# Kernel tuning notes

Hardware: AMD Instinct MI355X
Metric: run time of the kernel (lower is better)

Reference implementation:

```python
import jax, jax.numpy as jnp
import numpy as np

B, C_IN, C_OUT, N = 8, 256, 128, 4096
BN_EPS = 1e-5


def _conv1x1(w, b, t):
    # w: [out, in], t: [B, in, N] -> [B, out, N]
    return jnp.einsum('oc,bcn->bon', w, t) + b[None, :, None]


def setup_inputs() -> dict:
    key = jax.random.key(0)
    ks = jax.random.split(key, 11)
    s_in = 1.0 / np.sqrt(C_IN)
    s_out = 1.0 / np.sqrt(C_OUT)
    return {
        'x': jax.random.normal(ks[0], (B, C_IN, N), dtype=jnp.float32),
        'g_w': jax.random.normal(ks[1], (C_OUT, C_IN), dtype=jnp.float32) * s_in,
        'g_b': jax.random.normal(ks[2], (C_OUT,), dtype=jnp.float32) * s_in,
        'theta_w': jax.random.normal(ks[3], (C_OUT, C_IN), dtype=jnp.float32) * s_in,
        'theta_b': jax.random.normal(ks[4], (C_OUT,), dtype=jnp.float32) * s_in,
        'phi_w': jax.random.normal(ks[5], (C_OUT, C_IN), dtype=jnp.float32) * s_in,
        'phi_b': jax.random.normal(ks[6], (C_OUT,), dtype=jnp.float32) * s_in,
        'W_w': jax.random.normal(ks[7], (C_IN, C_OUT), dtype=jnp.float32) * s_out,
        'W_b': jax.random.normal(ks[8], (C_IN,), dtype=jnp.float32) * s_out,
        'bn_gamma': jax.random.uniform(ks[9], (C_IN,), dtype=jnp.float32),
        'bn_beta': jax.random.normal(ks[10], (C_IN,), dtype=jnp.float32) * 0.1,
    }


def reference(x, g_w, g_b, theta_w, theta_b, phi_w, phi_b, W_w, W_b, bn_gamma, bn_beta):
    n = x.shape[-1]
    g_x = _conv1x1(g_w, g_b, x)          # [B, Co, N]
    theta_x = _conv1x1(theta_w, theta_b, x)  # [B, Co, N]
    phi_x = _conv1x1(phi_w, phi_b, x)        # [B, Co, N]
    # f = theta_x^T @ phi_x, divided by N (no softmax) -> [B, N, N]
    f_div_c = jnp.einsum('bcn,bcm->bnm', theta_x, phi_x) / n
    # y[b,c,n] = sum_m f[b,n,m] * g_x[b,c,m]  -> already permuted to [B, Co, N]
    y = jnp.einsum('bnm,bcm->bcn', f_div_c, g_x)
    w_y = jnp.einsum('oc,bcn->bon', W_w, y) + W_b[None, :, None]  # [B, C_in, N]
    # BatchNorm1d, training mode: stats over (batch, spatial), biased variance
    mean = w_y.mean(axis=(0, 2), keepdims=True)
    var = w_y.var(axis=(0, 2), keepdims=True)
    w_y = (w_y - mean) * jax.lax.rsqrt(var + BN_EPS)
    w_y = w_y * bn_gamma[None, :, None] + bn_beta[None, :, None]
    return w_y + x  # generate=True residual
```

## Files before the change

kernel.cpp:

```cpp
#include <hip/hip_runtime.h>
#include <hip/hip_bf16.h>
#include <stdint.h>

#define BB   8
#define CIN  256
#define COUT 128
#define NN   4096

using f32x4  = __attribute__((ext_vector_type(4))) float;
using bf16x8 = __attribute__((ext_vector_type(8))) __bf16;
using u16x8  = __attribute__((ext_vector_type(8))) unsigned short;

static __device__ __forceinline__ unsigned short f2bf(float f) {
    unsigned int u = __builtin_bit_cast(unsigned int, f);
    u += 0x7FFFu + ((u >> 16) & 1u);
    return (unsigned short)(u >> 16);
}
static __device__ __forceinline__ float bf2f(unsigned short u) {
    return __builtin_bit_cast(float, (unsigned int)u << 16);
}
static __device__ __forceinline__ ushort4 pack4(float a, float b, float c, float d) {
    ushort4 r; r.x=f2bf(a); r.y=f2bf(b); r.z=f2bf(c); r.w=f2bf(d); return r;
}
static __device__ __forceinline__ bf16x8 pack8(float4 a, float4 b) {
    u16x8 r;
    r[0]=f2bf(a.x); r[1]=f2bf(a.y); r[2]=f2bf(a.z); r[3]=f2bf(a.w);
    r[4]=f2bf(b.x); r[5]=f2bf(b.y); r[6]=f2bf(b.z); r[7]=f2bf(b.w);
    return __builtin_bit_cast(bf16x8, r);
}
#define MFMA(a,b,c) __builtin_amdgcn_mfma_f32_16x16x32_bf16((a),(b),(c),0,0,0)

static __device__ __forceinline__ int sw64(int r, int c)  { return (r*64  + c) ^ ((r&7)<<3); }

typedef __attribute__((address_space(3))) unsigned int lds_uint;
typedef __attribute__((address_space(1))) const unsigned int glob_uint;
static __device__ __forceinline__ void glds16(const void* g, void* l) {
    __builtin_amdgcn_global_load_lds((glob_uint*)g, (lds_uint*)l, 16, 0, 0);
}

__global__ __launch_bounds__(256) void z0_prep(
    const float* __restrict__ gw, const float* __restrict__ pw, const float* __restrict__ tw,
    const float* __restrict__ gb, const float* __restrict__ pb, const float* __restrict__ tb,
    float* __restrict__ stats,
    unsigned short* __restrict__ Wcat, float* __restrict__ biascat)
{
    int t = blockIdx.x * 256 + threadIdx.x;
    int gs = gridDim.x * 256;
    for (int i = t; i < 24576; i += gs) {
        int flat = i * 4;
        int o = flat >> 8, c = flat & 255;
        const float* src = (o < 128) ? (gw + o*256) : (o < 256) ? (pw + (o-128)*256) : (tw + (o-256)*256);
        float4 f = *(const float4*)(src + c);
        ushort4 u; u.x=f2bf(f.x); u.y=f2bf(f.y); u.z=f2bf(f.z); u.w=f2bf(f.w);
        *(ushort4*)(Wcat + flat) = u;
    }
    if (t < 512) stats[t] = 0.f;
    if (t < 384)
        biascat[t] = (t < 128) ? gb[t] : (t < 256) ? pb[t-128] : tb[t-256];
}

__global__ __launch_bounds__(512) void k1_conv3(
    const float* __restrict__ x, const unsigned short* __restrict__ Wcat,
    const float* __restrict__ biascat,
    unsigned short* __restrict__ G, unsigned short* __restrict__ P,
    unsigned short* __restrict__ TT)
{
    __shared__ __align__(16) unsigned short Xs[128*256];
    int b  = blockIdx.x >> 5;
    int n0 = (blockIdx.x & 31) * 128;
    int t  = threadIdx.x;

    {
        int nq = (t & 31) * 4;
        int c0 = (t >> 5) * 4;
        const float* xb = x + (size_t)b*CIN*NN + n0 + nq;
        #pragma unroll
        for (int p = 0; p < 4; ++p) {
            int c = p*64 + c0;
            const float* xp = xb + (size_t)c*NN;
            float4 f0 = *(const float4*)(xp);
            float4 f1 = *(const float4*)(xp + NN);
            float4 f2 = *(const float4*)(xp + 2*NN);
            float4 f3 = *(const float4*)(xp + 3*NN);
            *(ushort4*)&Xs[(nq+0)*256 + (c ^ (((nq+0)&7)<<3))] = pack4(f0.x,f1.x,f2.x,f3.x);
            *(ushort4*)&Xs[(nq+1)*256 + (c ^ (((nq+1)&7)<<3))] = pack4(f0.y,f1.y,f2.y,f3.y);
            *(ushort4*)&Xs[(nq+2)*256 + (c ^ (((nq+2)&7)<<3))] = pack4(f0.z,f1.z,f2.z,f3.z);
            *(ushort4*)&Xs[(nq+3)*256 + (c ^ (((nq+3)&7)<<3))] = pack4(f0.w,f1.w,f2.w,f3.w);
        }
    }
    __syncthreads();

    int lane = t & 63, wv = t >> 6;
    int wr = wv >> 2, wc = wv & 3;
    int lr = lane & 15, lg = lane >> 4;
    int nb = wr*64, ob = wc*96;

    f32x4 acc[4][6];
    #pragma unroll
    for (int i=0;i<4;i++)
        #pragma unroll
        for (int j=0;j<6;j++) acc[i][j] = (f32x4){0.f,0.f,0.f,0.f};

    #pragma unroll
    for (int ks = 0; ks < 8; ++ks) {
        bf16x8 xf[4], wf[6];
        #pragma unroll
        for (int ni = 0; ni < 4; ++ni) {
            int n = nb + ni*16 + lr;
            int cq = (ks*4 + lg) ^ (n & 7);
            xf[ni] = __builtin_bit_cast(bf16x8, *(const u16x8*)&Xs[n*256 + cq*8]);
        }
        #pragma unroll
        for (int os = 0; os < 6; ++os) {
            int o = ob + os*16 + lr;
            wf[os] = __builtin_bit_cast(bf16x8, *(const u16x8*)(Wcat + (size_t)o*256 + ks*32 + lg*8));
        }
        #pragma unroll
        for (int os = 0; os < 6; ++os) {
            bool th = (ob + os*16) >= 256;
            #pragma unroll
            for (int ni = 0; ni < 4; ++ni)
                acc[ni][os] = th ? MFMA(wf[os], xf[ni], acc[ni][os])
                                 : MFMA(xf[ni], wf[os], acc[ni][os]);
        }
    }

    unsigned short* Gb  = G  + (size_t)b*COUT*NN;
    unsigned short* Pb  = P  + (size_t)b*COUT*NN;
    unsigned short* TTb = TT + (size_t)b*NN*COUT;
    #pragma unroll
    for (int os = 0; os < 6; ++os) {
        int o = ob + os*16;
        if (o < 256) {
            float bv = biascat[o + lr];
            unsigned short* dst = ((o < 128) ? (Gb + (size_t)(o + lr)*NN)
                                             : (Pb + (size_t)(o - 128 + lr)*NN)) + n0 + nb;
            #pragma unroll
            for (int ni = 0; ni < 4; ++ni) {
                f32x4 v = acc[ni][os];
                *(ushort4*)(dst + ni*16 + lg*4) = pack4(v[0]+bv, v[1]+bv, v[2]+bv, v[3]+bv);
            }
        } else {
            int c0 = o - 256 + lg*4;
            float b0 = biascat[o + lg*4 + 0];
            float b1 = biascat[o + lg*4 + 1];
            float b2 = biascat[o + lg*4 + 2];
            float b3 = biascat[o + lg*4 + 3];
            #pragma unroll
            for (int ni = 0; ni < 4; ++ni) {
                int n = n0 + nb + ni*16 + lr;
                f32x4 v = acc[ni][os];
                *(ushort4*)(TTb + (size_t)n*COUT + c0) = pack4(v[0]+b0, v[1]+b1, v[2]+b2, v[3]+b3);
            }
        }
    }
}

__global__ __launch_bounds__(256) void k2_m1(
    const unsigned short* __restrict__ P, const unsigned short* __restrict__ G,
    float* __restrict__ M1p)
{
    __shared__ __align__(16) unsigned short Ps[128*64];
    __shared__ __align__(16) unsigned short Gs[128*64];
    int bid = blockIdx.x;
    int b  = bid >> 4;
    int ks = bid & 15;
    int t = threadIdx.x;
    int lane = t & 63, wv = t >> 6;
    int wr = wv >> 1, wc = wv & 1;
    int lr = lane & 15, lg = lane >> 4;

    f32x4 acc[4][4];
    #pragma unroll
    for (int i=0;i<4;i++)
        #pragma unroll
        for (int j=0;j<4;j++) acc[i][j] = (f32x4){0.f,0.f,0.f,0.f};

    const unsigned short* Pb = P + (size_t)b*COUT*NN;
    const unsigned short* Gb = G + (size_t)b*COUT*NN;

    for (int it = 0; it < 4; ++it) {
        int n0 = ks*256 + it*64;
        #pragma unroll
        for (int g4 = 0; g4 < 4; ++g4) {
            int row0 = wv*32 + g4*8;
            int row  = row0 + (lane >> 3);
            int gg   = (lane & 7) ^ (row & 7);
            glds16(Pb + (size_t)row*NN + n0 + gg*8, &Ps[row0*64]);
            glds16(Gb + (size_t)row*NN + n0 + gg*8, &Gs[row0*64]);
        }
        asm volatile("s_waitcnt vmcnt(0)");
        __syncthreads();
        #pragma unroll
        for (int kk = 0; kk < 2; ++kk) {
            bf16x8 af[4], bfr[4];
            #pragma unroll
            for (int mi=0; mi<4; ++mi) {
                int row = wr*64 + mi*16 + lr;
                af[mi] = __builtin_bit_cast(bf16x8, *(const u16x8*)&Ps[sw64(row, kk*32 + lg*8)]);
            }
            #pragma unroll
            for (int ni=0; ni<4; ++ni) {
                int row = wc*64 + ni*16 + lr;
                bfr[ni] = __builtin_bit_cast(bf16x8, *(const u16x8*)&Gs[sw64(row, kk*32 + lg*8)]);
            }
            #pragma unroll
            for (int mi=0; mi<4; ++mi)
                #pragma unroll
                for (int ni=0; ni<4; ++ni)
                    acc[mi][ni] = MFMA(af[mi], bfr[ni], acc[mi][ni]);
        }
        __syncthreads();
    }
    float* dst = M1p + (size_t)bid*16384;
    #pragma unroll
    for (int mi=0; mi<4; ++mi)
        #pragma unroll
        for (int j=0; j<4; ++j) {
            int kch = wr*64 + mi*16 + lg*4 + j;
            #pragma unroll
            for (int ni=0; ni<4; ++ni) {
                int cch = wc*64 + ni*16 + lr;
                dst[kch*128 + cch] = acc[mi][ni][j];
            }
        }
}

__global__ __launch_bounds__(512) void k3_w2(
    const float* __restrict__ Ww, const float* __restrict__ M1p,
    unsigned short* __restrict__ W2)
{
    __shared__ float Ms[16384];
    int b = blockIdx.x;
    int t = threadIdx.x;

    for (int i4 = t; i4 < 4096; i4 += 512) {
        float4 s = {0.f,0.f,0.f,0.f};
        #pragma unroll
        for (int p = 0; p < 16; ++p) {
            float4 v = ((const float4*)(M1p + (size_t)(b*16 + p)*16384))[i4];
            s.x += v.x; s.y += v.y; s.z += v.z; s.w += v.w;
        }
        int k = i4 >> 5, q = i4 & 31;
        *(float4*)&Ms[k*128 + ((q ^ (k&7)) * 4)] = s;
    }
    __syncthreads();

    int lane = t & 63, wv = t >> 6;
    int lr = lane & 15, lg = lane >> 4;
    #pragma unroll
    for (int oo = 0; oo < 2; ++oo) {
        int o16 = oo*128 + wv*16;
        bf16x8 a[4];
        const float* wrow = Ww + (size_t)(o16 + lr)*128;
        #pragma unroll
        for (int ksx=0; ksx<4; ++ksx) {
            float4 f0 = *(const float4*)(wrow + ksx*32 + lg*8);
            float4 f1 = *(const float4*)(wrow + ksx*32 + lg*8 + 4);
            a[ksx] = pack8(f0, f1);
        }
        for (int kt = 0; kt < 8; ++kt) {
            f32x4 acc = (f32x4){0.f,0.f,0.f,0.f};
            int k = kt*16 + lr;
            #pragma unroll
            for (int ksx=0; ksx<4; ++ksx) {
                int q0 = ksx*8 + lg*2;
                float4 f0 = *(const float4*)&Ms[k*128 + ((q0     ^ (k&7)) * 4)];
                float4 f1 = *(const float4*)&Ms[k*128 + (((q0+1) ^ (k&7)) * 4)];
                acc = MFMA(a[ksx], pack8(f0, f1), acc);
            }
            #pragma unroll
            for (int j=0;j<4;++j) {
                int o = o16 + lg*4 + j;
                W2[(size_t)b*32768 + (size_t)o*128 + (kt*16 + lr)] = f2bf(acc[j] * (1.0f/4096.0f));
            }
        }
    }
}

__global__ __launch_bounds__(512) void k4_wy(
    const unsigned short* __restrict__ W2, const unsigned short* __restrict__ TT,
    const float* __restrict__ Wb, unsigned short* __restrict__ WY,
    float* __restrict__ stats)
{
    __shared__ __align__(16) unsigned short Ts[128*128];
    __shared__ float sb[512];
    int b  = blockIdx.x >> 5;
    int n0 = (blockIdx.x & 31) * 128;
    int t  = threadIdx.x;
    int lane = t & 63, wv = t >> 6;
    sb[t] = 0.f;

    const unsigned short* TTb = TT + ((size_t)b*NN + n0)*COUT;
    #pragma unroll
    for (int g = 0; g < 4; ++g) {
        int nl = wv*16 + g*4 + (lane >> 4);
        int kq = lane & 15;
        const unsigned short* src = TTb + (size_t)nl*128 + ((kq ^ (nl & 7)) * 8);
        glds16(src, &Ts[(wv*16 + g*4) * 128]);
    }
    asm volatile("s_waitcnt vmcnt(0)");
    __syncthreads();

    int wr = wv >> 2, wo = wv & 3;
    int lr = lane & 15, lg = lane >> 4;
    int nb = wr*64, ob = wo*64;
    const unsigned short* W2b = W2 + (size_t)b*32768;

    f32x4 acc[4][4];
    #pragma unroll
    for (int i=0;i<4;i++)
        #pragma unroll
        for (int j=0;j<4;j++) acc[i][j] = (f32x4){0.f,0.f,0.f,0.f};

    #pragma unroll
    for (int ks = 0; ks < 4; ++ks) {
        bf16x8 tf[4], wf[4];
        #pragma unroll
        for (int ni = 0; ni < 4; ++ni) {
            int n = nb + ni*16 + lr;
            int kq = (ks*4 + lg) ^ (n & 7);
            tf[ni] = __builtin_bit_cast(bf16x8, *(const u16x8*)&Ts[n*128 + kq*8]);
        }
        #pragma unroll
        for (int oi = 0; oi < 4; ++oi) {
            int o = ob + oi*16 + lr;
            wf[oi] = __builtin_bit_cast(bf16x8, *(const u16x8*)(W2b + (size_t)o*128 + ks*32 + lg*8));
        }
        #pragma unroll
        for (int ni = 0; ni < 4; ++ni)
            #pragma unroll
            for (int oi = 0; oi < 4; ++oi)
                acc[ni][oi] = MFMA(tf[ni], wf[oi], acc[ni][oi]);
    }

    unsigned short* wyb = WY + (size_t)b*CIN*NN;
    #pragma unroll
    for (int oi = 0; oi < 4; ++oi) {
        int o = ob + oi*16 + lr;
        float bv = Wb[o];
        float s1 = 0.f, s2 = 0.f;
        #pragma unroll
        for (int ni = 0; ni < 4; ++ni) {
            f32x4 v = acc[ni][oi];
            float v0 = v[0]+bv, v1 = v[1]+bv, v2 = v[2]+bv, v3 = v[3]+bv;
            s1 += v0+v1+v2+v3;
            s2 += v0*v0+v1*v1+v2*v2+v3*v3;
            *(ushort4*)(wyb + (size_t)o*NN + n0 + nb + ni*16 + lg*4) = pack4(v0,v1,v2,v3);
        }
        s1 += __shfl_xor(s1, 16); s1 += __shfl_xor(s1, 32);
        s2 += __shfl_xor(s2, 16); s2 += __shfl_xor(s2, 32);
        if (lg == 0) {
            atomicAdd(&sb[o], s1);
            atomicAdd(&sb[256 + o], s2);
        }
    }
    __syncthreads();
    atomicAdd(&stats[t], sb[t]);
}

__global__ __launch_bounds__(256) void k6_final(
    const unsigned short* __restrict__ WY, const float* __restrict__ x,
    const float* __restrict__ stats, const float* __restrict__ gamma,
    const float* __restrict__ beta, float* __restrict__ out)
{
    const float inv = 1.0f / (float)(BB * NN);
    int stride = gridDim.x * blockDim.x;
    for (int i = blockIdx.x * blockDim.x + threadIdx.x; i < (BB*CIN*NN)/8; i += stride) {
        int c = (i >> 9) & 255;
        float mean = stats[c] * inv;
        float var  = stats[256 + c] * inv - mean*mean;
        float sc   = gamma[c] * rsqrtf(var + 1e-5f);
        float bb   = beta[c];
        u16x8 w = ((const u16x8*)WY)[i];
        float4 x0 = ((const float4*)x)[i*2];
        float4 x1 = ((const float4*)x)[i*2+1];
        float4 r0, r1;
        r0.x = (bf2f(w[0]) - mean)*sc + bb + x0.x;
        r0.y = (bf2f(w[1]) - mean)*sc + bb + x0.y;
        r0.z = (bf2f(w[2]) - mean)*sc + bb + x0.z;
        r0.w = (bf2f(w[3]) - mean)*sc + bb + x0.w;
        r1.x = (bf2f(w[4]) - mean)*sc + bb + x1.x;
        r1.y = (bf2f(w[5]) - mean)*sc + bb + x1.y;
        r1.z = (bf2f(w[6]) - mean)*sc + bb + x1.z;
        r1.w = (bf2f(w[7]) - mean)*sc + bb + x1.w;
        ((float4*)out)[i*2]   = r0;
        ((float4*)out)[i*2+1] = r1;
    }
}

extern "C" void kernel_launch(void* const* d_in, const int* in_sizes, int n_in,
                              void* d_out, int out_size, void* d_ws, size_t ws_size,
                              hipStream_t stream)
{
    (void)in_sizes; (void)n_in; (void)out_size; (void)ws_size;
    const float* x     = (const float*)d_in[0];
    const float* gw    = (const float*)d_in[1];
    const float* gb    = (const float*)d_in[2];
    const float* tw    = (const float*)d_in[3];
    const float* tb    = (const float*)d_in[4];
    const float* pw    = (const float*)d_in[5];
    const float* pb    = (const float*)d_in[6];
    const float* Ww    = (const float*)d_in[7];
    const float* Wb    = (const float*)d_in[8];
    const float* gamma = (const float*)d_in[9];
    const float* beta  = (const float*)d_in[10];
    float* out = (float*)d_out;

    char* ws = (char*)d_ws;
    unsigned short* G    = (unsigned short*)(ws + 0);
    unsigned short* P    = (unsigned short*)(ws + (8u<<20));
    unsigned short* WY   = (unsigned short*)(ws + 0);
    unsigned short* TT   = (unsigned short*)(ws + (16u<<20));
    float* M1p           = (float*)(ws + (24u<<20));
    unsigned short* W2   = (unsigned short*)(ws + (32u<<20));
    unsigned short* Wcat = (unsigned short*)(ws + (33u<<20));
    float* biascat       = (float*)(ws + (33u<<20) + 196608);
    float* stats         = (float*)(ws + (33u<<20) + 198656);

    z0_prep <<<96,   256, 0, stream>>>(gw, pw, tw, gb, pb, tb, stats, Wcat, biascat);
    k1_conv3<<<256,  512, 0, stream>>>(x, Wcat, biascat, G, P, TT);
    k2_m1   <<<128,  256, 0, stream>>>(P, G, M1p);
    k3_w2   <<<8,    512, 0, stream>>>(Ww, M1p, W2);
    k4_wy   <<<256,  512, 0, stream>>>(W2, TT, Wb, WY, stats);
    k6_final<<<2048, 256, 0, stream>>>(WY, x, stats, gamma, beta, out);
}
```

Before: 96.35 us.

## Refactor nonlocal block via per-batch Gram matrix of x and closed-form BN stats

Replaces the conv/attention pipeline with an algebraic reformulation. Each batch's Gram matrix X·Xᵀ and channel sums of x are computed once. All 1x1 weights are folded into a single per-batch 256x256 effective matrix E, so the output becomes E·x plus a bias. BatchNorm statistics are derived analytically from E, the Gram matrix and the row sums, so no intermediate activation tensor is written. This removes the large G/P/TT/WY round trips, at the cost of fp32 partial-Gram traffic and a serial 8-block small-matrix stage, with different bf16 rounding behavior.

```diff
diff --git a/kernel.cpp b/kernel.cpp
--- a/kernel.cpp
+++ b/kernel.cpp
@@ -22,57 +22,397 @@
 static __device__ __forceinline__ ushort4 pack4(float a, float b, float c, float d) {
     ushort4 r; r.x=f2bf(a); r.y=f2bf(b); r.z=f2bf(c); r.w=f2bf(d); return r;
 }
-static __device__ __forceinline__ bf16x8 pack8(float4 a, float4 b) {
-    u16x8 r;
-    r[0]=f2bf(a.x); r[1]=f2bf(a.y); r[2]=f2bf(a.z); r[3]=f2bf(a.w);
-    r[4]=f2bf(b.x); r[5]=f2bf(b.y); r[6]=f2bf(b.z); r[7]=f2bf(b.w);
-    return __builtin_bit_cast(bf16x8, r);
-}
 #define MFMA(a,b,c) __builtin_amdgcn_mfma_f32_16x16x32_bf16((a),(b),(c),0,0,0)
 
-static __device__ __forceinline__ int sw64(int r, int c)  { return (r*64  + c) ^ ((r&7)<<3); }
-
-typedef __attribute__((address_space(3))) unsigned int lds_uint;
-typedef __attribute__((address_space(1))) const unsigned int glob_uint;
-static __device__ __forceinline__ void glds16(const void* g, void* l) {
-    __builtin_amdgcn_global_load_lds((glob_uint*)g, (lds_uint*)l, 16, 0, 0);
-}
-
-__global__ __launch_bounds__(256) void z0_prep(
-    const float* __restrict__ gw, const float* __restrict__ pw, const float* __restrict__ tw,
-    const float* __restrict__ gb, const float* __restrict__ pb, const float* __restrict__ tb,
-    float* __restrict__ stats,
-    unsigned short* __restrict__ Wcat, float* __restrict__ biascat)
+__global__ __launch_bounds__(512) void kA_gram(
+    const float* __restrict__ x, float* __restrict__ Sp, float* __restrict__ Rp)
 {
-    int t = blockIdx.x * 256 + threadIdx.x;
-    int gs = gridDim.x * 256;
-    for (int i = t; i < 24576; i += gs) {
-        int flat = i * 4;
-        int o = flat >> 8, c = flat & 255;
-        const float* src = (o < 128) ? (gw + o*256) : (o < 256) ? (pw + (o-128)*256) : (tw + (o-256)*256);
-        float4 f = *(const float4*)(src + c);
-        ushort4 u; u.x=f2bf(f.x); u.y=f2bf(f.y); u.z=f2bf(f.z); u.w=f2bf(f.w);
-        *(ushort4*)(Wcat + flat) = u;
-    }
-    if (t < 512) stats[t] = 0.f;
-    if (t < 384)
-        biascat[t] = (t < 128) ? gb[t] : (t < 256) ? pb[t-128] : tb[t-256];
-}
-
-__global__ __launch_bounds__(512) void k1_conv3(
-    const float* __restrict__ x, const unsigned short* __restrict__ Wcat,
-    const float* __restrict__ biascat,
-    unsigned short* __restrict__ G, unsigned short* __restrict__ P,
-    unsigned short* __restrict__ TT)
+    __shared__ __align__(16) unsigned short Xs[256*256];
+    int bid = blockIdx.x;
+    int b = bid >> 4, ch = bid & 15;
+    int n0 = ch * 256;
+    int t = threadIdx.x, lane = t & 63, wv = t >> 6;
+
+    const float* xb = x + (size_t)b*CIN*NN + n0;
+    #pragma unroll
+    for (int i = 0; i < 32; ++i) {
+        int c = wv*32 + i;
+        float4 f = *(const float4*)(xb + (size_t)c*NN + lane*4);
+        float s = f.x + f.y + f.z + f.w;
+        #pragma unroll
+        for (int off = 1; off < 64; off <<= 1) s += __shfl_xor(s, off);
+        if (lane == 0) Rp[bid*256 + c] = s;
+        *(ushort4*)&Xs[(c*256 + lane*4) ^ ((c&7)<<3)] = pack4(f.x, f.y, f.z, f.w);
+    }
+    __syncthreads();
+
+    int wr = wv >> 1, wc = wv & 1;
+    int lr = lane & 15, lg = lane >> 4;
+    f32x4 acc[4][8];
+    #pragma unroll
+    for (int i = 0; i < 4; ++i)
+        #pragma unroll
+        for (int j = 0; j < 8; ++j) acc[i][j] = (f32x4){0.f,0.f,0.f,0.f};
+
+    #pragma unroll
+    for (int ks = 0; ks < 8; ++ks) {
+        bf16x8 af[4], bfr[8];
+        #pragma unroll
+        for (int mi = 0; mi < 4; ++mi) {
+            int row = wr*64 + mi*16 + lr;
+            af[mi] = __builtin_bit_cast(bf16x8, *(const u16x8*)&Xs[(row*256 + ks*32 + lg*8) ^ ((row&7)<<3)]);
+        }
+        #pragma unroll
+        for (int ni = 0; ni < 8; ++ni) {
+            int row = wc*128 + ni*16 + lr;
+            bfr[ni] = __builtin_bit_cast(bf16x8, *(const u16x8*)&Xs[(row*256 + ks*32 + lg*8) ^ ((row&7)<<3)]);
+        }
+        #pragma unroll
+        for (int mi = 0; mi < 4; ++mi)
+            #pragma unroll
+            for (int ni = 0; ni < 8; ++ni)
+                acc[mi][ni] = MFMA(af[mi], bfr[ni], acc[mi][ni]);
+    }
+
+    float* dst = Sp + (size_t)bid * 65536;
+    #pragma unroll
+    for (int mi = 0; mi < 4; ++mi)
+        #pragma unroll
+        for (int ni = 0; ni < 8; ++ni)
+            #pragma unroll
+            for (int j = 0; j < 4; ++j) {
+                int c1 = wr*64 + mi*16 + lg*4 + j;
+                int c2 = wc*128 + ni*16 + lr;
+                dst[c1*256 + c2] = acc[mi][ni][j];
+            }
+}
+
+__global__ __launch_bounds__(256) void kR(
+    const float* __restrict__ Sp, const float* __restrict__ Rp,
+    const float* __restrict__ pw, const float* __restrict__ gw,
+    const float* __restrict__ tw, const float* __restrict__ Www,
+    unsigned short* __restrict__ Sbf, float* __restrict__ rv,
+    unsigned short* __restrict__ Pwb, unsigned short* __restrict__ Gwb,
+    unsigned short* __restrict__ TwT, unsigned short* __restrict__ Wwb,
+    float* __restrict__ stats)
+{
+    int blk = blockIdx.x, t = threadIdx.x;
+    if (blk < 128) {
+        int b = blk >> 4, part = blk & 15;
+        int base = part * 4096;
+        #pragma unroll
+        for (int i4 = t; i4 < 1024; i4 += 256) {
+            float4 s = {0.f,0.f,0.f,0.f};
+            #pragma unroll
+            for (int p = 0; p < 16; ++p) {
+                float4 v = *(const float4*)(Sp + (size_t)(b*16+p)*65536 + base + i4*4);
+                s.x += v.x; s.y += v.y; s.z += v.z; s.w += v.w;
+            }
+            *(ushort4*)(Sbf + (size_t)b*65536 + base + i4*4) = pack4(s.x, s.y, s.z, s.w);
+        }
+    } else if (blk < 136) {
+        int b = blk - 128;
+        float s = 0.f;
+        #pragma unroll
+        for (int p = 0; p < 16; ++p) s += Rp[(b*16+p)*256 + t];
+        rv[b*256 + t] = s;
+    } else {
+        int j = (blk - 136)*256 + t;
+        for (int i = j; i < 32768; i += 2048) {
+            Pwb[i] = f2bf(pw[i]);
+            Gwb[i] = f2bf(gw[i]);
+            Wwb[i] = f2bf(Www[i]);
+            int c = i >> 7, k = i & 127;
+            TwT[i] = f2bf(tw[k*256 + c]);
+        }
+        if (blk == 136) stats[t] = 0.f;
+        if (blk == 137) stats[256 + t] = 0.f;
+    }
+}
+
+__global__ __launch_bounds__(512) void kB12(
+    const unsigned short* __restrict__ Sbf, const float* __restrict__ rv,
+    const float* __restrict__ pwf, const float* __restrict__ gwf,
+    const unsigned short* __restrict__ Pwb, const unsigned short* __restrict__ Gwb,
+    const unsigned short* __restrict__ TwT, const unsigned short* __restrict__ Wwb,
+    const float* __restrict__ gbv, const float* __restrict__ pbv,
+    const float* __restrict__ tbv, const float* __restrict__ Wbv,
+    unsigned short* __restrict__ Ebf, float* __restrict__ fv)
+{
+    __shared__ __align__(16) unsigned short Ss[128*256];
+    __shared__ __align__(16) unsigned short Tbuf[128*128];
+    __shared__ float u_l[128], v_l[128], pb_l[128], gb_l[128];
+    int b = blockIdx.x, t = threadIdx.x, lane = t & 63, wv = t >> 6;
+    int lr = lane & 15, lg = lane >> 4;
+    const unsigned short* Sb = Sbf + (size_t)b*65536;
+    const float* rb = rv + b*256;
+
+    if (t < 128) {
+        float s = 0.f;
+        for (int c = 0; c < 256; ++c) s += pwf[t*256 + c] * rb[c];
+        u_l[t] = s; pb_l[t] = pbv[t];
+    } else if (t < 256) {
+        int k = t - 128;
+        float s = 0.f;
+        for (int c = 0; c < 256; ++c) s += gwf[k*256 + c] * rb[c];
+        v_l[k] = s; gb_l[k] = gbv[k];
+    }
+
+    int wrM = wv >> 2, wcM = wv & 3;
+    f32x4 accM[4][2];
+    #pragma unroll
+    for (int i = 0; i < 4; ++i) { accM[i][0] = (f32x4){0,0,0,0}; accM[i][1] = (f32x4){0,0,0,0}; }
+
+    for (int h = 0; h < 2; ++h) {
+        __syncthreads();
+        for (int i = t; i < 4096; i += 512) {
+            int row = i >> 5, c8 = (i & 31) * 8;
+            u16x8 vv = *(const u16x8*)(Sb + (size_t)(h*128 + row)*256 + c8);
+            *(u16x8*)&Ss[(row*256 + c8) ^ ((row&7)<<3)] = vv;
+        }
+        __syncthreads();
+        f32x4 accT[4][2];
+        #pragma unroll
+        for (int i = 0; i < 4; ++i) { accT[i][0] = (f32x4){0,0,0,0}; accT[i][1] = (f32x4){0,0,0,0}; }
+        #pragma unroll
+        for (int ks = 0; ks < 8; ++ks) {
+            bf16x8 a4[4], b2[2];
+            #pragma unroll
+            for (int mi = 0; mi < 4; ++mi) {
+                int k = wrM*64 + mi*16 + lr;
+                a4[mi] = __builtin_bit_cast(bf16x8, *(const u16x8*)(Pwb + (size_t)k*256 + ks*32 + lg*8));
+            }
+            #pragma unroll
+            for (int ni = 0; ni < 2; ++ni) {
+                int c2l = wcM*32 + ni*16 + lr;
+                b2[ni] = __builtin_bit_cast(bf16x8, *(const u16x8*)&Ss[(c2l*256 + ks*32 + lg*8) ^ ((c2l&7)<<3)]);
+            }
+            #pragma unroll
+            for (int mi = 0; mi < 4; ++mi)
+                #pragma unroll
+                for (int ni = 0; ni < 2; ++ni)
+                    accT[mi][ni] = MFMA(a4[mi], b2[ni], accT[mi][ni]);
+        }
+        __syncthreads();
+        #pragma unroll
+        for (int mi = 0; mi < 4; ++mi)
+            #pragma unroll
+            for (int ni = 0; ni < 2; ++ni)
+                #pragma unroll
+                for (int j = 0; j < 4; ++j) {
+                    int k = wrM*64 + mi*16 + lg*4 + j;
+                    int c2l = wcM*32 + ni*16 + lr;
+                    Tbuf[(k*128 + c2l) ^ ((k&7)<<3)] = f2bf(accT[mi][ni][j]);
+                }
+        __syncthreads();
+        #pragma unroll
+        for (int ks = 0; ks < 4; ++ks) {
+            bf16x8 a4[4], b2[2];
+            #pragma unroll
+            for (int mi = 0; mi < 4; ++mi) {
+                int k = wrM*64 + mi*16 + lr;
+                a4[mi] = __builtin_bit_cast(bf16x8, *(const u16x8*)&Tbuf[(k*128 + ks*32 + lg*8) ^ ((k&7)<<3)]);
+            }
+            #pragma unroll
+            for (int ni = 0; ni < 2; ++ni) {
+                int c = wcM*32 + ni*16 + lr;
+                b2[ni] = __builtin_bit_cast(bf16x8, *(const u16x8*)(Gwb + (size_t)c*256 + h*128 + ks*32 + lg*8));
+            }
+            #pragma unroll
+            for (int mi = 0; mi < 4; ++mi)
+                #pragma unroll
+                for (int ni = 0; ni < 2; ++ni)
+                    accM[mi][ni] = MFMA(a4[mi], b2[ni], accM[mi][ni]);
+        }
+    }
+    __syncthreads();
+    #pragma unroll
+    for (int mi = 0; mi < 4; ++mi)
+        #pragma unroll
+        for (int ni = 0; ni < 2; ++ni)
+            #pragma unroll
+            for (int j = 0; j < 4; ++j) {
+                int k = wrM*64 + mi*16 + lg*4 + j;
+                int c = wcM*32 + ni*16 + lr;
+                float val = accM[mi][ni][j] + u_l[k]*gb_l[c] + pb_l[k]*v_l[c] + 4096.0f*pb_l[k]*gb_l[c];
+                Tbuf[(k*128 + c) ^ ((k&7)<<3)] = f2bf(val);
+            }
+    __syncthreads();
+    int wrW = wv >> 1, wcW = wv & 1;
+    f32x4 accW[4][4];
+    #pragma unroll
+    for (int i = 0; i < 4; ++i)
+        #pragma unroll
+        for (int j = 0; j < 4; ++j) accW[i][j] = (f32x4){0,0,0,0};
+    #pragma unroll
+    for (int ks = 0; ks < 4; ++ks) {
+        bf16x8 a4[4], b4[4];
+        #pragma unroll
+        for (int mi = 0; mi < 4; ++mi) {
+            int o = wrW*64 + mi*16 + lr;
+            a4[mi] = __builtin_bit_cast(bf16x8, *(const u16x8*)(Wwb + (size_t)o*128 + ks*32 + lg*8));
+        }
+        #pragma unroll
+        for (int ni = 0; ni < 4; ++ni) {
+            int kk = wcW*64 + ni*16 + lr;
+            b4[ni] = __builtin_bit_cast(bf16x8, *(const u16x8*)&Tbuf[(kk*128 + ks*32 + lg*8) ^ ((kk&7)<<3)]);
+        }
+        #pragma unroll
+        for (int mi = 0; mi < 4; ++mi)
+            #pragma unroll
+            for (int ni = 0; ni < 4; ++ni)
+                accW[mi][ni] = MFMA(a4[mi], b4[ni], accW[mi][ni]);
+    }
+    __syncthreads();
+    #pragma unroll
+    for (int mi = 0; mi < 4; ++mi)
+        #pragma unroll
+        for (int ni = 0; ni < 4; ++ni)
+            #pragma unroll
+            for (int j = 0; j < 4; ++j) {
+                int o = wrW*64 + mi*16 + lg*4 + j;
+                int kk = wcW*64 + ni*16 + lr;
+                Ss[(o*128 + kk) ^ ((o&7)<<3)] = f2bf(accW[mi][ni][j] * (1.0f/4096.0f));
+            }
+    __syncthreads();
+    f32x4 accE[4][8];
+    #pragma unroll
+    for (int i = 0; i < 4; ++i)
+        #pragma unroll
+        for (int j = 0; j < 8; ++j) accE[i][j] = (f32x4){0,0,0,0};
+    #pragma unroll
+    for (int ks = 0; ks < 4; ++ks) {
+        bf16x8 a4[4], b8[8];
+        #pragma unroll
+        for (int mi = 0; mi < 4; ++mi) {
+            int o = wrW*64 + mi*16 + lr;
+            a4[mi] = __builtin_bit_cast(bf16x8, *(const u16x8*)&Ss[(o*128 + ks*32 + lg*8) ^ ((o&7)<<3)]);
+        }
+        #pragma unroll
+        for (int ni = 0; ni < 8; ++ni) {
+            int cp = wcW*128 + ni*16 + lr;
+            b8[ni] = __builtin_bit_cast(bf16x8, *(const u16x8*)(TwT + (size_t)cp*128 + ks*32 + lg*8));
+        }
+        #pragma unroll
+        for (int mi = 0; mi < 4; ++mi)
+            #pragma unroll
+            for (int ni = 0; ni < 8; ++ni)
+                accE[mi][ni] = MFMA(a4[mi], b8[ni], accE[mi][ni]);
+    }
+    unsigned short* Eb = Ebf + (size_t)b*65536;
+    #pragma unroll
+    for (int mi = 0; mi < 4; ++mi)
+        #pragma unroll
+        for (int ni = 0; ni < 8; ++ni)
+            #pragma unroll
+            for (int j = 0; j < 4; ++j) {
+                int o = wrW*64 + mi*16 + lg*4 + j;
+                int cp = wcW*128 + ni*16 + lr;
+                Eb[(size_t)o*256 + cp] = f2bf(accE[mi][ni][j]);
+            }
+    if (t < 256) {
+        float s = 0.f;
+        for (int kk = 0; kk < 128; ++kk)
+            s += bf2f(Ss[(t*128 + kk) ^ ((t&7)<<3)]) * tbv[kk];
+        fv[b*256 + t] = s + Wbv[t];
+    }
+}
+
+__global__ __launch_bounds__(256) void kB3(
+    const unsigned short* __restrict__ Ebf, const unsigned short* __restrict__ Sbf,
+    const float* __restrict__ rv, const float* __restrict__ fv, float* __restrict__ stats)
+{
+    __shared__ __align__(16) unsigned short Es[64*256];
+    __shared__ float s2l[64];
+    __shared__ float er4[256];
+    int b = blockIdx.x >> 2, sl = blockIdx.x & 3, obase = sl*64;
+    int t = threadIdx.x, lane = t & 63, wv = t >> 6, lr = lane & 15, lg = lane >> 4;
+    const unsigned short* Eb = Ebf + (size_t)b*65536;
+    const unsigned short* Sb = Sbf + (size_t)b*65536;
+
+    for (int i = t; i < 2048; i += 256) {
+        int row = i >> 5, c8 = (i & 31) * 8;
+        u16x8 vv = *(const u16x8*)(Eb + (size_t)(obase + row)*256 + c8);
+        *(u16x8*)&Es[(row*256 + c8) ^ ((row&7)<<3)] = vv;
+    }
+    if (t < 64) s2l[t] = 0.f;
+    __syncthreads();
+
+    f32x4 acc[4][4];
+    #pragma unroll
+    for (int i = 0; i < 4; ++i)
+        #pragma unroll
+        for (int j = 0; j < 4; ++j) acc[i][j] = (f32x4){0,0,0,0};
+    #pragma unroll
+    for (int ks = 0; ks < 8; ++ks) {
+        bf16x8 a4[4], b4[4];
+        #pragma unroll
+        for (int mi = 0; mi < 4; ++mi) {
+            int ol = mi*16 + lr;
+            a4[mi] = __builtin_bit_cast(bf16x8, *(const u16x8*)&Es[(ol*256 + ks*32 + lg*8) ^ ((ol&7)<<3)]);
+        }
+        #pragma unroll
+        for (int ni = 0; ni < 4; ++ni) {
+            int c2 = wv*64 + ni*16 + lr;
+            b4[ni] = __builtin_bit_cast(bf16x8, *(const u16x8*)(Sb + (size_t)c2*256 + ks*32 + lg*8));
+        }
+        #pragma unroll
+        for (int mi = 0; mi < 4; ++mi)
+            #pragma unroll
+            for (int ni = 0; ni < 4; ++ni)
+                acc[mi][ni] = MFMA(a4[mi], b4[ni], acc[mi][ni]);
+    }
+    #pragma unroll
+    for (int mi = 0; mi < 4; ++mi)
+        #pragma unroll
+        for (int j = 0; j < 4; ++j) {
+            int ol = mi*16 + lg*4 + j;
+            float v = 0.f;
+            #pragma unroll
+            for (int ni = 0; ni < 4; ++ni) {
+                int c2 = wv*64 + ni*16 + lr;
+                v += acc[mi][ni][j] * bf2f(Es[(ol*256 + c2) ^ ((ol&7)<<3)]);
+            }
+            v += __shfl_xor(v, 1); v += __shfl_xor(v, 2);
+            v += __shfl_xor(v, 4); v += __shfl_xor(v, 8);
+            if (lr == 0) atomicAdd(&s2l[ol], v);
+        }
+    {
+        int ol = t & 63, q = t >> 6;
+        float p = 0.f;
+        for (int c = q*64; c < q*64 + 64; ++c)
+            p += bf2f(Es[(ol*256 + c) ^ ((ol&7)<<3)]) * rv[b*256 + c];
+        er4[q*64 + ol] = p;
+    }
+    __syncthreads();
+    if (t < 64) {
+        float er = er4[t] + er4[64+t] + er4[128+t] + er4[192+t];
+        float fo = fv[b*256 + obase + t];
+        atomicAdd(&stats[obase + t], er + 4096.0f*fo);
+        atomicAdd(&stats[256 + obase + t], s2l[t] + 2.0f*fo*er + 4096.0f*fo*fo);
+    }
+}
+
+__global__ __launch_bounds__(512) void kF(
+    const float* __restrict__ x, const unsigned short* __restrict__ Ebf,
+    const float* __restrict__ fv, const float* __restrict__ stats,
+    const float* __restrict__ gamma, const float* __restrict__ beta,
+    float* __restrict__ out)
 {
     __shared__ __align__(16) unsigned short Xs[128*256];
-    int b  = blockIdx.x >> 5;
-    int n0 = (blockIdx.x & 31) * 128;
-    int t  = threadIdx.x;
-
+    __shared__ float scale_l[256], shift_l[256];
+    int b = blockIdx.x >> 5, n0 = (blockIdx.x & 31) * 128;
+    int t = threadIdx.x, lane = t & 63, wv = t >> 6, lr = lane & 15, lg = lane >> 4;
+    const float inv = 1.0f / 32768.0f;
+    if (t < 256) {
+        float mu  = stats[t] * inv;
+        float var = stats[256 + t] * inv - mu*mu;
+        float sc  = gamma[t] * rsqrtf(var + 1e-5f);
+        scale_l[t] = sc;
+        shift_l[t] = (fv[b*256 + t] - mu) * sc + beta[t];
+    }
     {
-        int nq = (t & 31) * 4;
-        int c0 = (t >> 5) * 4;
+        int nq = (t & 31) * 4, c0 = (t >> 5) * 4;
         const float* xb = x + (size_t)b*CIN*NN + n0 + nq;
         #pragma unroll
         for (int p = 0; p < 4; ++p) {
@@ -90,302 +430,52 @@
     }
     __syncthreads();
 
-    int lane = t & 63, wv = t >> 6;
-    int wr = wv >> 2, wc = wv & 3;
-    int lr = lane & 15, lg = lane >> 4;
-    int nb = wr*64, ob = wc*96;
-
-    f32x4 acc[4][6];
-    #pragma unroll
-    for (int i=0;i<4;i++)
-        #pragma unroll
-        for (int j=0;j<6;j++) acc[i][j] = (f32x4){0.f,0.f,0.f,0.f};
+    int wn = wv >> 2, wo = wv & 3;
+    int nb = wn*64, ob = wo*64;
+    const unsigned short* Eb = Ebf + (size_t)b*65536;
+    f32x4 acc[4][4];
+    #pragma unroll
+    for (int i = 0; i < 4; ++i)
+        #pragma unroll
+        for (int j = 0; j < 4; ++j) acc[i][j] = (f32x4){0,0,0,0};
 
     #pragma unroll
     for (int ks = 0; ks < 8; ++ks) {
-        bf16x8 xf[4], wf[6];
+        bf16x8 xf[4], ef[4];
         #pragma unroll
         for (int ni = 0; ni < 4; ++ni) {
             int n = nb + ni*16 + lr;
-            int cq = (ks*4 + lg) ^ (n & 7);
-            xf[ni] = __builtin_bit_cast(bf16x8, *(const u16x8*)&Xs[n*256 + cq*8]);
-        }
-        #pragma unroll
-        for (int os = 0; os < 6; ++os) {
-            int o = ob + os*16 + lr;
-            wf[os] = __builtin_bit_cast(bf16x8, *(const u16x8*)(Wcat + (size_t)o*256 + ks*32 + lg*8));
-        }
-        #pragma unroll
-        for (int os = 0; os < 6; ++os) {
-            bool th = (ob + os*16) >= 256;
-            #pragma unroll
-            for (int ni = 0; ni < 4; ++ni)
-                acc[ni][os] = th ? MFMA(wf[os], xf[ni], acc[ni][os])
-                                 : MFMA(xf[ni], wf[os], acc[ni][os]);
-        }
-    }
-
-    unsigned short* Gb  = G  + (size_t)b*COUT*NN;
-    unsigned short* Pb  = P  + (size_t)b*COUT*NN;
-    unsigned short* TTb = TT + (size_t)b*NN*COUT;
-    #pragma unroll
-    for (int os = 0; os < 6; ++os) {
-        int o = ob + os*16;
-        if (o < 256) {
-            float bv = biascat[o + lr];
-            unsigned short* dst = ((o < 128) ? (Gb + (size_t)(o + lr)*NN)
-                                             : (Pb + (size_t)(o - 128 + lr)*NN)) + n0 + nb;
-            #pragma unroll
-            for (int ni = 0; ni < 4; ++ni) {
-                f32x4 v = acc[ni][os];
-                *(ushort4*)(dst + ni*16 + lg*4) = pack4(v[0]+bv, v[1]+bv, v[2]+bv, v[3]+bv);
-            }
-        } else {
-            int c0 = o - 256 + lg*4;
-            float b0 = biascat[o + lg*4 + 0];
-            float b1 = biascat[o + lg*4 + 1];
-            float b2 = biascat[o + lg*4 + 2];
-            float b3 = biascat[o + lg*4 + 3];
-            #pragma unroll
-            for (int ni = 0; ni < 4; ++ni) {
-                int n = n0 + nb + ni*16 + lr;
-                f32x4 v = acc[ni][os];
-                *(ushort4*)(TTb + (size_t)n*COUT + c0) = pack4(v[0]+b0, v[1]+b1, v[2]+b2, v[3]+b3);
-            }
-        }
-    }
-}
-
-__global__ __launch_bounds__(256) void k2_m1(
-    const unsigned short* __restrict__ P, const unsigned short* __restrict__ G,
-    float* __restrict__ M1p)
-{
-    __shared__ __align__(16) unsigned short Ps[128*64];
-    __shared__ __align__(16) unsigned short Gs[128*64];
-    int bid = blockIdx.x;
-    int b  = bid >> 4;
-    int ks = bid & 15;
-    int t = threadIdx.x;
-    int lane = t & 63, wv = t >> 6;
-    int wr = wv >> 1, wc = wv & 1;
-    int lr = lane & 15, lg = lane >> 4;
-
-    f32x4 acc[4][4];
-    #pragma unroll
-    for (int i=0;i<4;i++)
-        #pragma unroll
-        for (int j=0;j<4;j++) acc[i][j] = (f32x4){0.f,0.f,0.f,0.f};
-
-    const unsigned short* Pb = P + (size_t)b*COUT*NN;
-    const unsigned short* Gb = G + (size_t)b*COUT*NN;
-
-    for (int it = 0; it < 4; ++it) {
-        int n0 = ks*256 + it*64;
-        #pragma unroll
-        for (int g4 = 0; g4 < 4; ++g4) {
-            int row0 = wv*32 + g4*8;
-            int row  = row0 + (lane >> 3);
-            int gg   = (lane & 7) ^ (row & 7);
-            glds16(Pb + (size_t)row*NN + n0 + gg*8, &Ps[row0*64]);
-            glds16(Gb + (size_t)row*NN + n0 + gg*8, &Gs[row0*64]);
-        }
-        asm volatile("s_waitcnt vmcnt(0)");
-        __syncthreads();
-        #pragma unroll
-        for (int kk = 0; kk < 2; ++kk) {
-            bf16x8 af[4], bfr[4];
-            #pragma unroll
-            for (int mi=0; mi<4; ++mi) {
-                int row = wr*64 + mi*16 + lr;
-                af[mi] = __builtin_bit_cast(bf16x8, *(const u16x8*)&Ps[sw64(row, kk*32 + lg*8)]);
-            }
-            #pragma unroll
-            for (int ni=0; ni<4; ++ni) {
-                int row = wc*64 + ni*16 + lr;
-                bfr[ni] = __builtin_bit_cast(bf16x8, *(const u16x8*)&Gs[sw64(row, kk*32 + lg*8)]);
-            }
-            #pragma unroll
-            for (int mi=0; mi<4; ++mi)
-                #pragma unroll
-                for (int ni=0; ni<4; ++ni)
-                    acc[mi][ni] = MFMA(af[mi], bfr[ni], acc[mi][ni]);
-        }
-        __syncthreads();
-    }
-    float* dst = M1p + (size_t)bid*16384;
-    #pragma unroll
-    for (int mi=0; mi<4; ++mi)
-        #pragma unroll
-        for (int j=0; j<4; ++j) {
-            int kch = wr*64 + mi*16 + lg*4 + j;
-            #pragma unroll
-            for (int ni=0; ni<4; ++ni) {
-                int cch = wc*64 + ni*16 + lr;
-                dst[kch*128 + cch] = acc[mi][ni][j];
-            }
-        }
-}
-
-__global__ __launch_bounds__(512) void k3_w2(
-    const float* __restrict__ Ww, const float* __restrict__ M1p,
-    unsigned short* __restrict__ W2)
-{
-    __shared__ float Ms[16384];
-    int b = blockIdx.x;
-    int t = threadIdx.x;
-
-    for (int i4 = t; i4 < 4096; i4 += 512) {
-        float4 s = {0.f,0.f,0.f,0.f};
-        #pragma unroll
-        for (int p = 0; p < 16; ++p) {
-            float4 v = ((const float4*)(M1p + (size_t)(b*16 + p)*16384))[i4];
-            s.x += v.x; s.y += v.y; s.z += v.z; s.w += v.w;
-        }
-        int k = i4 >> 5, q = i4 & 31;
-        *(float4*)&Ms[k*128 + ((q ^ (k&7)) * 4)] = s;
-    }
-    __syncthreads();
-
-    int lane = t & 63, wv = t >> 6;
-    int lr = lane & 15, lg = lane >> 4;
-    #pragma unroll
-    for (int oo = 0; oo < 2; ++oo) {
-        int o16 = oo*128 + wv*16;
-        bf16x8 a[4];
-        const float* wrow = Ww + (size_t)(o16 + lr)*128;
-        #pragma unroll
-        for (int ksx=0; ksx<4; ++ksx) {
-            float4 f0 = *(const float4*)(wrow + ksx*32 + lg*8);
-            float4 f1 = *(const float4*)(wrow + ksx*32 + lg*8 + 4);
-            a[ksx] = pack8(f0, f1);
-        }
-        for (int kt = 0; kt < 8; ++kt) {
-            f32x4 acc = (f32x4){0.f,0.f,0.f,0.f};
-            int k = kt*16 + lr;
-            #pragma unroll
-            for (int ksx=0; ksx<4; ++ksx) {
-                int q0 = ksx*8 + lg*2;
-                float4 f0 = *(const float4*)&Ms[k*128 + ((q0     ^ (k&7)) * 4)];
-                float4 f1 = *(const float4*)&Ms[k*128 + (((q0+1) ^ (k&7)) * 4)];
-                acc = MFMA(a[ksx], pack8(f0, f1), acc);
-            }
-            #pragma unroll
-            for (int j=0;j<4;++j) {
-                int o = o16 + lg*4 + j;
-                W2[(size_t)b*32768 + (size_t)o*128 + (kt*16 + lr)] = f2bf(acc[j] * (1.0f/4096.0f));
-            }
-        }
-    }
-}
-
-__global__ __launch_bounds__(512) void k4_wy(
-    const unsigned short* __restrict__ W2, const unsigned short* __restrict__ TT,
-    const float* __restrict__ Wb, unsigned short* __restrict__ WY,
-    float* __restrict__ stats)
-{
-    __shared__ __align__(16) unsigned short Ts[128*128];
-    __shared__ float sb[512];
-    int b  = blockIdx.x >> 5;
-    int n0 = (blockIdx.x & 31) * 128;
-    int t  = threadIdx.x;
-    int lane = t & 63, wv = t >> 6;
-    sb[t] = 0.f;
-
-    const unsigned short* TTb = TT + ((size_t)b*NN + n0)*COUT;
-    #pragma unroll
-    for (int g = 0; g < 4; ++g) {
-        int nl = wv*16 + g*4 + (lane >> 4);
-        int kq = lane & 15;
-        const unsigned short* src = TTb + (size_t)nl*128 + ((kq ^ (nl & 7)) * 8);
-        glds16(src, &Ts[(wv*16 + g*4) * 128]);
-    }
-    asm volatile("s_waitcnt vmcnt(0)");
-    __syncthreads();
-
-    int wr = wv >> 2, wo = wv & 3;
-    int lr = lane & 15, lg = lane >> 4;
-    int nb = wr*64, ob = wo*64;
-    const unsigned short* W2b = W2 + (size_t)b*32768;
-
-    f32x4 acc[4][4];
-    #pragma unroll
-    for (int i=0;i<4;i++)
-        #pragma unroll
-        for (int j=0;j<4;j++) acc[i][j] = (f32x4){0.f,0.f,0.f,0.f};
-
-    #pragma unroll
-    for (int ks = 0; ks < 4; ++ks) {
-        bf16x8 tf[4], wf[4];
-        #pragma unroll
-        for (int ni = 0; ni < 4; ++ni) {
-            int n = nb + ni*16 + lr;
-            int kq = (ks*4 + lg) ^ (n & 7);
-            tf[ni] = __builtin_bit_cast(bf16x8, *(const u16x8*)&Ts[n*128 + kq*8]);
+            xf[ni] = __builtin_bit_cast(bf16x8, *(const u16x8*)&Xs[(n*256 + ks*32 + lg*8) ^ ((n&7)<<3)]);
         }
         #pragma unroll
         for (int oi = 0; oi < 4; ++oi) {
             int o = ob + oi*16 + lr;
-            wf[oi] = __builtin_bit_cast(bf16x8, *(const u16x8*)(W2b + (size_t)o*128 + ks*32 + lg*8));
+            ef[oi] = __builtin_bit_cast(bf16x8, *(const u16x8*)(Eb + (size_t)o*256 + ks*32 + lg*8));
         }
         #pragma unroll
         for (int ni = 0; ni < 4; ++ni)
             #pragma unroll
             for (int oi = 0; oi < 4; ++oi)
-                acc[ni][oi] = MFMA(tf[ni], wf[oi], acc[ni][oi]);
-    }
-
-    unsigned short* wyb = WY + (size_t)b*CIN*NN;
+                acc[ni][oi] = MFMA(xf[ni], ef[oi], acc[ni][oi]);
+    }
+
+    float* op = out + (size_t)b*CIN*NN;
     #pragma unroll
     for (int oi = 0; oi < 4; ++oi) {
         int o = ob + oi*16 + lr;
-        float bv = Wb[o];
-        float s1 = 0.f, s2 = 0.f;
+        float sc = scale_l[o], sh = shift_l[o];
         #pragma unroll
         for (int ni = 0; ni < 4; ++ni) {
-            f32x4 v = acc[ni][oi];
-            float v0 = v[0]+bv, v1 = v[1]+bv, v2 = v[2]+bv, v3 = v[3]+bv;
-            s1 += v0+v1+v2+v3;
-            s2 += v0*v0+v1*v1+v2*v2+v3*v3;
-            *(ushort4*)(wyb + (size_t)o*NN + n0 + nb + ni*16 + lg*4) = pack4(v0,v1,v2,v3);
-        }
-        s1 += __shfl_xor(s1, 16); s1 += __shfl_xor(s1, 32);
-        s2 += __shfl_xor(s2, 16); s2 += __shfl_xor(s2, 32);
-        if (lg == 0) {
-            atomicAdd(&sb[o], s1);
-            atomicAdd(&sb[256 + o], s2);
-        }
-    }
-    __syncthreads();
-    atomicAdd(&stats[t], sb[t]);
-}
-
-__global__ __launch_bounds__(256) void k6_final(
-    const unsigned short* __restrict__ WY, const float* __restrict__ x,
-    const float* __restrict__ stats, const float* __restrict__ gamma,
-    const float* __restrict__ beta, float* __restrict__ out)
-{
-    const float inv = 1.0f / (float)(BB * NN);
-    int stride = gridDim.x * blockDim.x;
-    for (int i = blockIdx.x * blockDim.x + threadIdx.x; i < (BB*CIN*NN)/8; i += stride) {
-        int c = (i >> 9) & 255;
-        float mean = stats[c] * inv;
-        float var  = stats[256 + c] * inv - mean*mean;
-        float sc   = gamma[c] * rsqrtf(var + 1e-5f);
-        float bb   = beta[c];
-        u16x8 w = ((const u16x8*)WY)[i];
-        float4 x0 = ((const float4*)x)[i*2];
-        float4 x1 = ((const float4*)x)[i*2+1];
-        float4 r0, r1;
-        r0.x = (bf2f(w[0]) - mean)*sc + bb + x0.x;
-        r0.y = (bf2f(w[1]) - mean)*sc + bb + x0.y;
-        r0.z = (bf2f(w[2]) - mean)*sc + bb + x0.z;
-        r0.w = (bf2f(w[3]) - mean)*sc + bb + x0.w;
-        r1.x = (bf2f(w[4]) - mean)*sc + bb + x1.x;
-        r1.y = (bf2f(w[5]) - mean)*sc + bb + x1.y;
-        r1.z = (bf2f(w[6]) - mean)*sc + bb + x1.z;
-        r1.w = (bf2f(w[7]) - mean)*sc + bb + x1.w;
-        ((float4*)out)[i*2]   = r0;
-        ((float4*)out)[i*2+1] = r1;
+            int nbase = nb + ni*16 + lg*4;
+            float4 st;
+            float* sp = &st.x;
+            #pragma unroll
+            for (int j = 0; j < 4; ++j) {
+                int n = nbase + j;
+                sp[j] = acc[ni][oi][j]*sc + sh + bf2f(Xs[(n*256 + o) ^ ((n&7)<<3)]);
+            }
+            *(float4*)(op + (size_t)o*NN + n0 + nbase) = st;
+        }
     }
 }
 
@@ -408,20 +498,21 @@
     float* out = (float*)d_out;
 
     char* ws = (char*)d_ws;
-    unsigned short* G    = (unsigned short*)(ws + 0);
-    unsigned short* P    = (unsigned short*)(ws + (8u<<20));
-    unsigned short* WY   = (unsigned short*)(ws + 0);
-    unsigned short* TT   = (unsigned short*)(ws + (16u<<20));
-    float* M1p           = (float*)(ws + (24u<<20));
-    unsigned short* W2   = (unsigned short*)(ws + (32u<<20));
-    unsigned short* Wcat = (unsigned short*)(ws + (33u<<20));
-    float* biascat       = (float*)(ws + (33u<<20) + 196608);
-    float* stats         = (float*)(ws + (33u<<20) + 198656);
-
-    z0_prep <<<96,   256, 0, stream>>>(gw, pw, tw, gb, pb, tb, stats, Wcat, biascat);
-    k1_conv3<<<256,  512, 0, stream>>>(x, Wcat, biascat, G, P, TT);
-    k2_m1   <<<128,  256, 0, stream>>>(P, G, M1p);
-    k3_w2   <<<8,    512, 0, stream>>>(Ww, M1p, W2);
-    k4_wy   <<<256,  512, 0, stream>>>(W2, TT, Wb, WY, stats);
-    k6_final<<<2048, 256, 0, stream>>>(WY, x, stats, gamma, beta, out);
-}
+    float* Sp            = (float*)(ws + 0);
+    unsigned short* Sbf  = (unsigned short*)(ws + 33554432);
+    float* Rp            = (float*)(ws + 34603008);
+    float* rv            = (float*)(ws + 34734080);
+    unsigned short* Pwb  = (unsigned short*)(ws + 34742272);
+    unsigned short* Gwb  = (unsigned short*)(ws + 34807808);
+    unsigned short* TwT  = (unsigned short*)(ws + 34873344);
+    unsigned short* Wwb  = (unsigned short*)(ws + 34938880);
+    unsigned short* Ebf  = (unsigned short*)(ws + 35004416);
+    float* fv            = (float*)(ws + 36052992);
+    float* stats         = (float*)(ws + 36061184);
+
+    kA_gram<<<128, 512, 0, stream>>>(x, Sp, Rp);
+    kR     <<<144, 256, 0, stream>>>(Sp, Rp, pw, gw, tw, Ww, Sbf, rv, Pwb, Gwb, TwT, Wwb, stats);
+    kB12   <<<8,   512, 0, stream>>>(Sbf, rv, pw, gw, Pwb, Gwb, TwT, Wwb, gb, pb, tb, Wb, Ebf, fv);
+    kB3    <<<32,  256, 0, stream>>>(Ebf, Sbf, rv, fv, stats);
+    kF     <<<256, 512, 0, stream>>>(x, Ebf, fv, stats, gamma, beta, out);
+}
```

After: 134.4 us. +39.5%, slower.
